# Optimization experiments

Hardware: AMD Instinct MI355X
Metric: run time of the kernel (lower is better)

Reference implementation:

```python
import jax, jax.numpy as jnp
import numpy as np

D_MODEL = 512
NUM_HEADS = 8
HEAD_DIM = D_MODEL // NUM_HEADS
BATCH = 4
SEQ = 2048
ROPE_BASE = 10000.0


def rope_cos_sin(seq_len, head_dim):
    inv_freq = 1.0 / (ROPE_BASE ** (jnp.arange(0, head_dim, 2, dtype=jnp.float32) / head_dim))
    t = jnp.arange(seq_len, dtype=jnp.float32)
    freqs = jnp.outer(t, inv_freq)              # (S, head_dim/2)
    emb = jnp.concatenate([freqs, freqs], axis=-1)  # (S, head_dim)
    return jnp.cos(emb), jnp.sin(emb)


def apply_rope(x, cos, sin):
    # x: (..., S, head_dim); cos/sin: (S, head_dim)
    x1 = x[..., ::2]
    x2 = x[..., 1::2]
    ch = cos[..., ::2]
    sh = sin[..., ::2]
    r1 = x1 * ch - x2 * sh
    r2 = x1 * sh + x2 * ch
    return jnp.stack([r1, r2], axis=-1).reshape(x.shape)


def setup_inputs() -> dict:
    key = jax.random.key(0)
    ks = jax.random.split(key, 12)
    x = jax.random.normal(ks[0], (BATCH, SEQ, D_MODEL), dtype=jnp.float32)
    variate_ids = jnp.sort(jax.random.randint(ks[1], (BATCH, SEQ), 0, 8), axis=-1).astype(jnp.int64)
    mask = jnp.ones((BATCH, SEQ), dtype=jnp.float32)
    s = 1.0 / np.sqrt(D_MODEL)
    Wq = jax.random.normal(ks[2], (D_MODEL, D_MODEL), dtype=jnp.float32) * s
    bq = jnp.zeros((D_MODEL,), dtype=jnp.float32)
    Wk = jax.random.normal(ks[3], (D_MODEL, D_MODEL), dtype=jnp.float32) * s
    bk = jnp.zeros((D_MODEL,), dtype=jnp.float32)
    Wv = jax.random.normal(ks[4], (D_MODEL, D_MODEL), dtype=jnp.float32) * s
    bv = jnp.zeros((D_MODEL,), dtype=jnp.float32)
    Wo = jax.random.normal(ks[5], (D_MODEL, D_MODEL), dtype=jnp.float32) * s
    bo = jnp.zeros((D_MODEL,), dtype=jnp.float32)
    u_same = jax.random.normal(ks[6], (NUM_HEADS,), dtype=jnp.float32) * 0.1
    u_cross = jax.random.normal(ks[7], (NUM_HEADS,), dtype=jnp.float32) * 0.1
    return dict(x=x, variate_ids=variate_ids, mask=mask, Wq=Wq, bq=bq, Wk=Wk, bk=bk,
                Wv=Wv, bv=bv, Wo=Wo, bo=bo, u_same=u_same, u_cross=u_cross)


def reference(x, variate_ids, mask, Wq, bq, Wk, bk, Wv, bv, Wo, bo, u_same, u_cross):
    B, S, D = x.shape
    H, Hd = NUM_HEADS, HEAD_DIM
    scale = 1.0 / np.sqrt(Hd)

    def proj(W, b):
        return (x @ W.T + b).reshape(B, S, H, Hd).transpose(0, 2, 1, 3)  # (B,H,S,Hd)

    q = proj(Wq, bq)
    k = proj(Wk, bk)
    v = proj(Wv, bv)

    cos, sin = rope_cos_sin(S, Hd)
    q = apply_rope(q, cos, sin)
    k = apply_rope(k, cos, sin)

    scores = jnp.einsum('bhid,bhjd->bhij', q, k) * scale  # (B,H,S,S)
    same = (variate_ids[:, :, None] == variate_ids[:, None, :]).astype(jnp.float32)  # (B,S,S)
    bias = same[:, None] * u_same[None, :, None, None] + (1.0 - same)[:, None] * u_cross[None, :, None, None]
    scores = scores + bias
    scores = scores + (1.0 - mask[:, None, None, :]) * -1e9
    probs = jax.nn.softmax(scores, axis=-1)
    out = jnp.einsum('bhij,bhjd->bhid', probs, v)  # (B,H,S,Hd)
    out = out.transpose(0, 2, 1, 3).reshape(B, S, D)
    return out @ Wo.T + bo
```

## Files before the change

kernel.cpp:

```cpp
#include <hip/hip_runtime.h>

#define BATCH   4
#define SEQ     2048
#define DMODEL  512
#define NHEADS  8
#define HEADDIM 64
#define MTOT    (BATCH*SEQ)
#define NX      (MTOT*DMODEL)
#define NW      (DMODEL*DMODEL)
#define QTILE   128
#define KTILE   64
#define NKT     (SEQ/KTILE)

#define LOG2E   1.4426950408889634f
#define SCL2    0.18033688011112042f
#define SHIFT   14.426950408889634f

typedef unsigned short u16;
typedef __bf16 bf16x8 __attribute__((ext_vector_type(8)));
typedef float  f32x4  __attribute__((ext_vector_type(4)));
typedef unsigned short u16x4 __attribute__((ext_vector_type(4)));

#define MFMA(a,b,c) __builtin_amdgcn_mfma_f32_16x16x32_bf16(a,b,c,0,0,0)

__device__ __forceinline__ u16 f2bf(float f) {
    unsigned u = __float_as_uint(f);
    u += 0x7FFFu + ((u >> 16) & 1u);
    return (u16)(u >> 16);
}

__device__ __forceinline__ float qsum16(float v) {
    v += __shfl_xor(v, 1);
    v += __shfl_xor(v, 2);
    v += __shfl_xor(v, 4);
    v += __shfl_xor(v, 8);
    return v;
}

__device__ __forceinline__ void gll16(const void* g, void* l) {
    __builtin_amdgcn_global_load_lds((const __attribute__((address_space(1))) void*)g,
                                     (__attribute__((address_space(3))) void*)l, 16, 0, 0);
}
__device__ __forceinline__ void gll4(const void* g, void* l) {
    __builtin_amdgcn_global_load_lds((const __attribute__((address_space(1))) void*)g,
                                     (__attribute__((address_space(3))) void*)l, 4, 0, 0);
}

#define NCVT4 ((NX + 4*NW)/4)
__global__ __launch_bounds__(256) void cvt_rope_kernel(
    const float* __restrict__ x,
    const float* __restrict__ wq, const float* __restrict__ wk,
    const float* __restrict__ wv, const float* __restrict__ wo,
    u16* __restrict__ xbf,
    u16* __restrict__ wqbf, u16* __restrict__ wkbf,
    u16* __restrict__ wvbf, u16* __restrict__ wobf,
    float* __restrict__ cos_t, float* __restrict__ sin_t)
{
    int i4 = blockIdx.x * 256 + threadIdx.x;
    if (i4 < NCVT4) {
        int i = i4 * 4;
        const float* s; u16* d; int o;
        if (i < NX) { s = x; d = xbf; o = i; }
        else {
            int j = i - NX;
            int r = j >> 18;
            o = j & (NW - 1);
            s = (r == 0) ? wq : (r == 1) ? wk : (r == 2) ? wv : wo;
            d = (r == 0) ? wqbf : (r == 1) ? wkbf : (r == 2) ? wvbf : wobf;
        }
        float4 v = *(const float4*)(s + o);
        u16x4 u = { f2bf(v.x), f2bf(v.y), f2bf(v.z), f2bf(v.w) };
        *(u16x4*)(d + o) = u;
    } else {
        int r = i4 - NCVT4;
        if (r < SEQ * 32 / 4) {
            int idx = r * 4;
            int s  = idx >> 5;
            int p0 = idx & 31;
#pragma unroll
            for (int t = 0; t < 4; ++t) {
                int p = p0 + t;
                float inv = __expf(-0.5756462732485115f * (float)(p & 15));
                float ang = (float)s * inv;
                cos_t[idx + t] = cosf(ang);
                sin_t[idx + t] = sinf(ang);
            }
        }
    }
}

__global__ __launch_bounds__(256) void qkv_kernel(
    const u16* __restrict__ x,
    const u16* __restrict__ Wq, const float* __restrict__ bq,
    const u16* __restrict__ Wk, const float* __restrict__ bk,
    const u16* __restrict__ Wv, const float* __restrict__ bv,
    const float* __restrict__ cos_t, const float* __restrict__ sin_t,
    u16* __restrict__ qws, u16* __restrict__ kws, u16* __restrict__ vtws)
{
    __shared__ alignas(16) u16 As[128 * 64];
    __shared__ alignas(16) u16 Bs[128 * 64];

    const int m0 = blockIdx.x * 128;
    const int n0 = blockIdx.y * 128;
    const int tid  = threadIdx.x;
    const int w    = tid >> 6;
    const int lane = tid & 63;
    const int quad = lane >> 4;
    const int l16  = lane & 15;
    const int wm = w & 1, wn = w >> 1;

    const int sec = n0 >> 9;
    const int oc0 = n0 & 511;
    const u16*   Wm = (sec == 0) ? Wq : (sec == 1 ? Wk : Wv);
    const float* bb = (sec == 0) ? bq : (sec == 1 ? bk : bv);

    f32x4 acc[4][4] = {};

    for (int kb = 0; kb < 8; ++kb) {
#pragma unroll
        for (int it = 0; it < 4; ++it) {
            const int s   = it * 256 + tid;
            const int row = s >> 3;
            const int cb  = s & 7;
            const int gcol = kb * 64 + (((cb ^ (row & 7))) << 3);
            gll16(x  + (m0  + row) * 512 + gcol, &As[s * 8]);
            gll16(Wm + (oc0 + row) * 512 + gcol, &Bs[s * 8]);
        }
        __syncthreads();

#pragma unroll
        for (int ks = 0; ks < 2; ++ks) {
            bf16x8 a[4], bfr[4];
#pragma unroll
            for (int t = 0; t < 4; ++t) {
                const int arow = wm * 64 + t * 16 + l16;
                a[t]   = *(const bf16x8*)&As[arow * 64 + (((ks * 4 + quad) ^ (arow & 7)) << 3)];
                const int brow = wn * 64 + t * 16 + l16;
                bfr[t] = *(const bf16x8*)&Bs[brow * 64 + (((ks * 4 + quad) ^ (brow & 7)) << 3)];
            }
#pragma unroll
            for (int tm = 0; tm < 4; ++tm)
#pragma unroll
                for (int tn = 0; tn < 4; ++tn)
                    acc[tm][tn] = MFMA(a[tm], bfr[tn], acc[tm][tn]);
        }
        __syncthreads();
    }

#pragma unroll
    for (int tm = 0; tm < 4; ++tm) {
#pragma unroll
        for (int tn = 0; tn < 4; ++tn) {
            const int col = oc0 + wn * 64 + tn * 16 + l16;
            const int hh  = col >> 6;
            const int d   = col & 63;
            const float bval = bb[col];
#pragma unroll
            for (int r = 0; r < 4; ++r) {
                const int R = m0 + wm * 64 + tm * 16 + quad * 4 + r;
                const int bi = R >> 11;
                const int s  = R & 2047;
                const size_t hb = (size_t)(bi * NHEADS + hh) * (SEQ * HEADDIM);
                float val = acc[tm][tn][r] + bval;
                if (sec < 2) {
                    float other = __shfl_xor(val, 1);
                    const int p = d >> 1;
                    const float c  = cos_t[s * 32 + p];
                    const float sn = sin_t[s * 32 + p];
                    float res = ((d & 1) == 0) ? (val * c - other * sn)
                                               : (other * sn + val * c);
                    if (sec == 0) {
                        qws[hb + s * HEADDIM + d] = f2bf(res);
                    } else {
                        const int kt = s >> 6, sr = s & 63;
                        kws[hb + ((kt * 64 + sr) << 6)
                               + ((((d >> 3) ^ (sr & 7)) << 3) + (d & 7))] = f2bf(res);
                    }
                } else {
                    const int kt = s >> 6, sc = s & 63;
                    vtws[hb + ((kt * 64 + d) << 6)
                            + ((((sc >> 3) ^ (d & 7)) << 3) + (sc & 7))] = f2bf(val);
                }
            }
        }
    }
}

__global__ __launch_bounds__(512) void attn_kernel(
    const u16* __restrict__ qws, const u16* __restrict__ ktl,
    const u16* __restrict__ vtl,
    const int* __restrict__ vids, const float* __restrict__ mask,
    const float* __restrict__ u_same, const float* __restrict__ u_cross,
    u16* __restrict__ attn)
{
    __shared__ alignas(16) u16 kbuf[2][KTILE * 64];
    __shared__ alignas(16) u16 vbuf[2][KTILE * 64];
    __shared__ alignas(16) u16 pls[8][16][72];
    __shared__ int   bid[2][KTILE];
    __shared__ float bmk[2][KTILE];

    const int bh = blockIdx.y;
    const int b  = bh >> 3;
    const int h  = bh & 7;
    const int q0 = blockIdx.x * QTILE;

    const int tid  = threadIdx.x;
    const int w    = tid >> 6;
    const int lane = tid & 63;
    const int quad = lane >> 4;
    const int l16  = lane & 15;

    const float us2 = u_same[h]  * LOG2E;
    const float uc2 = u_cross[h] * LOG2E;
    const size_t tb = (size_t)bh * (SEQ * HEADDIM);

    const int qr = q0 + w * 16 + l16;
    const bf16x8 aq0 = *(const bf16x8*)(qws + tb + qr * HEADDIM + quad * 8);
    const bf16x8 aq1 = *(const bf16x8*)(qws + tb + qr * HEADDIM + 32 + quad * 8);

    int vq[4];
#pragma unroll
    for (int r = 0; r < 4; ++r)
        vq[r] = vids[b * SEQ + q0 + w * 16 + quad * 4 + r];

    float li[4] = {0.f, 0.f, 0.f, 0.f};
    f32x4 o[4] = {};

    auto stage = [&](int kt, int nb) {
        const u16* kg = ktl + tb + (size_t)kt * (KTILE * 64);
        const u16* vg = vtl + tb + (size_t)kt * (KTILE * 64);
        const int off = w * 512;
        gll16(kg + off + lane * 8, &kbuf[nb][off]);
        gll16(vg + off + lane * 8, &vbuf[nb][off]);
        if (w == 0) {
            gll4(vids + b * SEQ + kt * KTILE + lane, &bid[nb][0]);
            gll4(mask + b * SEQ + kt * KTILE + lane, &bmk[nb][0]);
        }
    };

    stage(0, 0);

    for (int kt = 0; kt < NKT; ++kt) {
        const int cur = kt & 1;
        __syncthreads();
        if (kt + 1 < NKT) stage(kt + 1, cur ^ 1);

#pragma unroll
        for (int nt = 0; nt < 4; ++nt) {
            const int krow = nt * 16 + l16;
            const int r7   = krow & 7;
            const bf16x8 kb0 = *(const bf16x8*)&kbuf[cur][krow * 64 + ((quad ^ r7) << 3)];
            const bf16x8 kb1 = *(const bf16x8*)&kbuf[cur][krow * 64 + ((quad ^ r7 ^ 4) << 3)];
            f32x4 sc = {};
            sc = MFMA(aq0, kb0, sc);
            sc = MFMA(aq1, kb1, sc);
            const int   kv  = bid[cur][krow];
            const float mdl = fmaf(1.0f - bmk[cur][krow], -1.4426950408889634e9f, -SHIFT);
#pragma unroll
            for (int r = 0; r < 4; ++r) {
                const float sel = (kv == vq[r]) ? us2 : uc2;
                const float p = exp2f(fmaf(sc[r], SCL2, sel + mdl));
                li[r] += p;
                pls[w][quad * 4 + r][nt * 16 + l16] = f2bf(p);
            }
        }

        const bf16x8 ap0 = *(const bf16x8*)&pls[w][l16][quad * 8];
        const bf16x8 ap1 = *(const bf16x8*)&pls[w][l16][32 + quad * 8];

#pragma unroll
        for (int nt = 0; nt < 4; ++nt) {
            const int vrow = nt * 16 + l16;
            const int r7   = vrow & 7;
            const bf16x8 vb0 = *(const bf16x8*)&vbuf[cur][vrow * 64 + ((quad ^ r7) << 3)];
            const bf16x8 vb1 = *(const bf16x8*)&vbuf[cur][vrow * 64 + ((quad ^ r7 ^ 4) << 3)];
            o[nt] = MFMA(ap0, vb0, o[nt]);
            o[nt] = MFMA(ap1, vb1, o[nt]);
        }
    }

#pragma unroll
    for (int r = 0; r < 4; ++r) {
        const float inv = 1.0f / qsum16(li[r]);
        const int R = q0 + w * 16 + quad * 4 + r;
        const int rb = (b * SEQ + R) * DMODEL + h * HEADDIM;
#pragma unroll
        for (int nt = 0; nt < 4; ++nt)
            attn[rb + nt * 16 + l16] = f2bf(o[nt][r] * inv);
    }
}

__global__ __launch_bounds__(256) void proj_kernel(
    const u16* __restrict__ a, const u16* __restrict__ Wo,
    const float* __restrict__ bo, float* __restrict__ out)
{
    __shared__ alignas(16) u16 As[128 * 64];
    __shared__ alignas(16) u16 Bs[128 * 64];

    const int m0 = blockIdx.x * 128;
    const int n0 = blockIdx.y * 128;
    const int tid  = threadIdx.x;
    const int w    = tid >> 6;
    const int lane = tid & 63;
    const int quad = lane >> 4;
    const int l16  = lane & 15;
    const int wm = w & 1, wn = w >> 1;

    f32x4 acc[4][4] = {};

    for (int kb = 0; kb < 8; ++kb) {
#pragma unroll
        for (int it = 0; it < 4; ++it) {
            const int s   = it * 256 + tid;
            const int row = s >> 3;
            const int cb  = s & 7;
            const int gcol = kb * 64 + (((cb ^ (row & 7))) << 3);
            gll16(a  + (m0 + row) * 512 + gcol, &As[s * 8]);
            gll16(Wo + (n0 + row) * 512 + gcol, &Bs[s * 8]);
        }
        __syncthreads();

#pragma unroll
        for (int ks = 0; ks < 2; ++ks) {
            bf16x8 av[4], bv[4];
#pragma unroll
            for (int t = 0; t < 4; ++t) {
                const int arow = wm * 64 + t * 16 + l16;
                av[t] = *(const bf16x8*)&As[arow * 64 + (((ks * 4 + quad) ^ (arow & 7)) << 3)];
                const int brow = wn * 64 + t * 16 + l16;
                bv[t] = *(const bf16x8*)&Bs[brow * 64 + (((ks * 4 + quad) ^ (brow & 7)) << 3)];
            }
#pragma unroll
            for (int tm = 0; tm < 4; ++tm)
#pragma unroll
                for (int tn = 0; tn < 4; ++tn)
                    acc[tm][tn] = MFMA(av[tm], bv[tn], acc[tm][tn]);
        }
        __syncthreads();
    }

#pragma unroll
    for (int tm = 0; tm < 4; ++tm) {
#pragma unroll
        for (int tn = 0; tn < 4; ++tn) {
            const int col = n0 + wn * 64 + tn * 16 + l16;
            const float bval = bo[col];
#pragma unroll
            for (int r = 0; r < 4; ++r) {
                const int R = m0 + wm * 64 + tm * 16 + quad * 4 + r;
                out[R * 512 + col] = acc[tm][tn][r] + bval;
            }
        }
    }
}

extern "C" void kernel_launch(void* const* d_in, const int* in_sizes, int n_in,
                              void* d_out, int out_size, void* d_ws, size_t ws_size,
                              hipStream_t stream) {
    const float* x    = (const float*)d_in[0];
    const int*   vids = (const int*)d_in[1];
    const float* mask = (const float*)d_in[2];
    const float* Wq = (const float*)d_in[3];
    const float* bq = (const float*)d_in[4];
    const float* Wk = (const float*)d_in[5];
    const float* bk = (const float*)d_in[6];
    const float* Wv = (const float*)d_in[7];
    const float* bv = (const float*)d_in[8];
    const float* Wo = (const float*)d_in[9];
    const float* bo = (const float*)d_in[10];
    const float* usame  = (const float*)d_in[11];
    const float* ucross = (const float*)d_in[12];
    float* out = (float*)d_out;

    u16* xbf  = (u16*)d_ws;
    u16* wqbf = xbf + NX;
    u16* wkbf = wqbf + NW;
    u16* wvbf = wkbf + NW;
    u16* wobf = wvbf + NW;
    float* cos_t = (float*)(wobf + NW);
    float* sin_t = cos_t + SEQ * 32;
    u16* qws  = (u16*)(sin_t + SEQ * 32);
    u16* kws  = qws + (size_t)BATCH * NHEADS * SEQ * HEADDIM;
    u16* vtws = kws + (size_t)BATCH * NHEADS * SEQ * HEADDIM;
    u16* attn = xbf;

    cvt_rope_kernel<<<(NCVT4 + SEQ * 32 / 4 + 255) / 256, 256, 0, stream>>>(
        x, Wq, Wk, Wv, Wo, xbf, wqbf, wkbf, wvbf, wobf, cos_t, sin_t);

    dim3 g1(MTOT / 128, 3 * DMODEL / 128);
    qkv_kernel<<<g1, 256, 0, stream>>>(xbf, wqbf, bq, wkbf, bk, wvbf, bv,
                                       cos_t, sin_t, qws, kws, vtws);

    dim3 g2(SEQ / QTILE, BATCH * NHEADS);
    attn_kernel<<<g2, 512, 0, stream>>>(qws, kws, vtws, vids, mask,
                                        usame, ucross, attn);

    dim3 g3(MTOT / 128, DMODEL / 128);
    proj_kernel<<<g3, 256, 0, stream>>>(attn, wobf, bo, out);
}
```

Baseline: 221.2 us.

## Store K/V in plain layout, swizzle on load, pack bf16 stores, unroll attention loop

The QKV epilogue now writes K row-major and V transposed as plain [d][seq], with packed bf16 conversions and a vectorized 8-byte store for V. The LDS swizzle moves into the attention kernel's global-to-LDS staging. Cos/sin are interleaved into one float2 table. The attention loop is unrolled by two with fixed double-buffer indices, the bias/mask add is precombined, P is packed with bf16x2 conversion, and launch bounds request 4 blocks per CU. The aim is cheaper epilogue stores and lower softmax ALU cost, at the risk of less coalesced strided K/V staging loads.

```diff
diff --git a/kernel.cpp b/kernel.cpp
--- a/kernel.cpp
+++ b/kernel.cpp
@@ -1,4 +1,5 @@
 #include <hip/hip_runtime.h>
+#include <hip/hip_bf16.h>
 
 #define BATCH   4
 #define SEQ     2048
@@ -20,6 +21,7 @@
 typedef __bf16 bf16x8 __attribute__((ext_vector_type(8)));
 typedef float  f32x4  __attribute__((ext_vector_type(4)));
 typedef unsigned short u16x4 __attribute__((ext_vector_type(4)));
+typedef unsigned u32x2 __attribute__((ext_vector_type(2)));
 
 #define MFMA(a,b,c) __builtin_amdgcn_mfma_f32_16x16x32_bf16(a,b,c,0,0,0)
 
@@ -27,6 +29,12 @@
     unsigned u = __float_as_uint(f);
     u += 0x7FFFu + ((u >> 16) & 1u);
     return (u16)(u >> 16);
+}
+
+__device__ __forceinline__ unsigned pk_bf16(float a, float b) {
+    union { __hip_bfloat162 h; unsigned u; } cv;
+    cv.h = __float22bfloat162_rn(make_float2(a, b));
+    return cv.u;
 }
 
 __device__ __forceinline__ float qsum16(float v) {
@@ -54,7 +62,7 @@
     u16* __restrict__ xbf,
     u16* __restrict__ wqbf, u16* __restrict__ wkbf,
     u16* __restrict__ wvbf, u16* __restrict__ wobf,
-    float* __restrict__ cos_t, float* __restrict__ sin_t)
+    float2* __restrict__ cst)
 {
     int i4 = blockIdx.x * 256 + threadIdx.x;
     if (i4 < NCVT4) {
@@ -82,8 +90,7 @@
                 int p = p0 + t;
                 float inv = __expf(-0.5756462732485115f * (float)(p & 15));
                 float ang = (float)s * inv;
-                cos_t[idx + t] = cosf(ang);
-                sin_t[idx + t] = sinf(ang);
+                cst[idx + t] = make_float2(cosf(ang), sinf(ang));
             }
         }
     }
@@ -94,7 +101,7 @@
     const u16* __restrict__ Wq, const float* __restrict__ bq,
     const u16* __restrict__ Wk, const float* __restrict__ bk,
     const u16* __restrict__ Wv, const float* __restrict__ bv,
-    const float* __restrict__ cos_t, const float* __restrict__ sin_t,
+    const float2* __restrict__ cst,
     u16* __restrict__ qws, u16* __restrict__ kws, u16* __restrict__ vtws)
 {
     __shared__ alignas(16) u16 As[128 * 64];
@@ -113,6 +120,7 @@
     const int oc0 = n0 & 511;
     const u16*   Wm = (sec == 0) ? Wq : (sec == 1 ? Wk : Wv);
     const float* bb = (sec == 0) ? bq : (sec == 1 ? bk : bv);
+    const float  sgn = (l16 & 1) ? 1.0f : -1.0f;
 
     f32x4 acc[4][4] = {};
 
@@ -149,45 +157,42 @@
 
 #pragma unroll
     for (int tm = 0; tm < 4; ++tm) {
+        const int R0 = m0 + wm * 64 + tm * 16 + quad * 4;
+        const int bi = R0 >> 11;
+        const int s0 = R0 & 2047;
 #pragma unroll
         for (int tn = 0; tn < 4; ++tn) {
             const int col = oc0 + wn * 64 + tn * 16 + l16;
             const int hh  = col >> 6;
             const int d   = col & 63;
             const float bval = bb[col];
-#pragma unroll
-            for (int r = 0; r < 4; ++r) {
-                const int R = m0 + wm * 64 + tm * 16 + quad * 4 + r;
-                const int bi = R >> 11;
-                const int s  = R & 2047;
-                const size_t hb = (size_t)(bi * NHEADS + hh) * (SEQ * HEADDIM);
-                float val = acc[tm][tn][r] + bval;
-                if (sec < 2) {
+            const size_t hb = (size_t)(bi * NHEADS + hh) * (SEQ * HEADDIM);
+            float res[4];
+            if (sec < 2) {
+#pragma unroll
+                for (int r = 0; r < 4; ++r) {
+                    float val = acc[tm][tn][r] + bval;
                     float other = __shfl_xor(val, 1);
-                    const int p = d >> 1;
-                    const float c  = cos_t[s * 32 + p];
-                    const float sn = sin_t[s * 32 + p];
-                    float res = ((d & 1) == 0) ? (val * c - other * sn)
-                                               : (other * sn + val * c);
-                    if (sec == 0) {
-                        qws[hb + s * HEADDIM + d] = f2bf(res);
-                    } else {
-                        const int kt = s >> 6, sr = s & 63;
-                        kws[hb + ((kt * 64 + sr) << 6)
-                               + ((((d >> 3) ^ (sr & 7)) << 3) + (d & 7))] = f2bf(res);
-                    }
-                } else {
-                    const int kt = s >> 6, sc = s & 63;
-                    vtws[hb + ((kt * 64 + d) << 6)
-                            + ((((sc >> 3) ^ (d & 7)) << 3) + (sc & 7))] = f2bf(val);
+                    float2 cs = cst[(s0 + r) * 32 + (d >> 1)];
+                    res[r] = fmaf(val, cs.x, other * (sgn * cs.y));
                 }
-            }
-        }
-    }
-}
-
-__global__ __launch_bounds__(512) void attn_kernel(
-    const u16* __restrict__ qws, const u16* __restrict__ ktl,
+                const unsigned p01 = pk_bf16(res[0], res[1]);
+                const unsigned p23 = pk_bf16(res[2], res[3]);
+                u16* dp = ((sec == 0) ? qws : kws) + hb + (size_t)s0 * HEADDIM + d;
+                dp[0]   = (u16)p01;  dp[64]  = (u16)(p01 >> 16);
+                dp[128] = (u16)p23;  dp[192] = (u16)(p23 >> 16);
+            } else {
+#pragma unroll
+                for (int r = 0; r < 4; ++r) res[r] = acc[tm][tn][r] + bval;
+                u32x2 pv = { pk_bf16(res[0], res[1]), pk_bf16(res[2], res[3]) };
+                *(u32x2*)(vtws + hb + (size_t)d * SEQ + s0) = pv;
+            }
+        }
+    }
+}
+
+__global__ __launch_bounds__(512, 4) void attn_kernel(
+    const u16* __restrict__ qws, const u16* __restrict__ kws,
     const u16* __restrict__ vtl,
     const int* __restrict__ vids, const float* __restrict__ mask,
     const float* __restrict__ u_same, const float* __restrict__ u_cross,
@@ -226,25 +231,20 @@
     float li[4] = {0.f, 0.f, 0.f, 0.f};
     f32x4 o[4] = {};
 
+    const int srow = w * 8 + (lane >> 3);
+    const int scb  = lane & 7;
+    const int soff = ((scb ^ (srow & 7)) << 3);
     auto stage = [&](int kt, int nb) {
-        const u16* kg = ktl + tb + (size_t)kt * (KTILE * 64);
-        const u16* vg = vtl + tb + (size_t)kt * (KTILE * 64);
-        const int off = w * 512;
-        gll16(kg + off + lane * 8, &kbuf[nb][off]);
-        gll16(vg + off + lane * 8, &vbuf[nb][off]);
+        const int k0 = kt * KTILE;
+        gll16(kws + tb + (size_t)(k0 + srow) * HEADDIM + soff, &kbuf[nb][w * 512 + (lane & 7) * 8 + ((lane >> 3) & 7) * 0 + lane * 8 - lane * 8 + (srow - w * 8) * 64 + scb * 8]);
+        gll16(vtl + tb + (size_t)srow * SEQ + k0 + soff,        &vbuf[nb][(srow - w * 8) * 64 + w * 512 + scb * 8]);
         if (w == 0) {
-            gll4(vids + b * SEQ + kt * KTILE + lane, &bid[nb][0]);
-            gll4(mask + b * SEQ + kt * KTILE + lane, &bmk[nb][0]);
+            gll4(vids + b * SEQ + k0 + lane, &bid[nb][0]);
+            gll4(mask + b * SEQ + k0 + lane, &bmk[nb][0]);
         }
     };
 
-    stage(0, 0);
-
-    for (int kt = 0; kt < NKT; ++kt) {
-        const int cur = kt & 1;
-        __syncthreads();
-        if (kt + 1 < NKT) stage(kt + 1, cur ^ 1);
-
+    auto body = [&](const int cur) {
 #pragma unroll
         for (int nt = 0; nt < 4; ++nt) {
             const int krow = nt * 16 + l16;
@@ -255,14 +255,22 @@
             sc = MFMA(aq0, kb0, sc);
             sc = MFMA(aq1, kb1, sc);
             const int   kv  = bid[cur][krow];
-            const float mdl = fmaf(1.0f - bmk[cur][krow], -1.4426950408889634e9f, -SHIFT);
+            const float mdl = fmaf(bmk[cur][krow], 1.4426950408889634e9f,
+                                   -1.4426950408889634e9f - SHIFT);
+            const float as_ = us2 + mdl;
+            const float ac_ = uc2 + mdl;
+            float p[4];
 #pragma unroll
             for (int r = 0; r < 4; ++r) {
-                const float sel = (kv == vq[r]) ? us2 : uc2;
-                const float p = exp2f(fmaf(sc[r], SCL2, sel + mdl));
-                li[r] += p;
-                pls[w][quad * 4 + r][nt * 16 + l16] = f2bf(p);
-            }
+                const float sel = (kv == vq[r]) ? as_ : ac_;
+                p[r] = exp2f(fmaf(sc[r], SCL2, sel));
+                li[r] += p[r];
+            }
+            const unsigned p01 = pk_bf16(p[0], p[1]);
+            const unsigned p23 = pk_bf16(p[2], p[3]);
+            u16* pb = &pls[w][quad * 4][nt * 16 + l16];
+            pb[0]       = (u16)p01;  pb[72]      = (u16)(p01 >> 16);
+            pb[2 * 72]  = (u16)p23;  pb[3 * 72]  = (u16)(p23 >> 16);
         }
 
         const bf16x8 ap0 = *(const bf16x8*)&pls[w][l16][quad * 8];
@@ -277,6 +285,16 @@
             o[nt] = MFMA(ap0, vb0, o[nt]);
             o[nt] = MFMA(ap1, vb1, o[nt]);
         }
+    };
+
+    stage(0, 0);
+    for (int kt = 0; kt < NKT; kt += 2) {
+        __syncthreads();
+        stage(kt + 1, 1);
+        body(0);
+        __syncthreads();
+        if (kt + 2 < NKT) stage(kt + 2, 0);
+        body(1);
     }
 
 #pragma unroll
@@ -377,19 +395,18 @@
     u16* wkbf = wqbf + NW;
     u16* wvbf = wkbf + NW;
     u16* wobf = wvbf + NW;
-    float* cos_t = (float*)(wobf + NW);
-    float* sin_t = cos_t + SEQ * 32;
-    u16* qws  = (u16*)(sin_t + SEQ * 32);
+    float2* cst = (float2*)(wobf + NW);
+    u16* qws  = (u16*)(cst + SEQ * 32);
     u16* kws  = qws + (size_t)BATCH * NHEADS * SEQ * HEADDIM;
     u16* vtws = kws + (size_t)BATCH * NHEADS * SEQ * HEADDIM;
     u16* attn = xbf;
 
     cvt_rope_kernel<<<(NCVT4 + SEQ * 32 / 4 + 255) / 256, 256, 0, stream>>>(
-        x, Wq, Wk, Wv, Wo, xbf, wqbf, wkbf, wvbf, wobf, cos_t, sin_t);
+        x, Wq, Wk, Wv, Wo, xbf, wqbf, wkbf, wvbf, wobf, cst);
 
     dim3 g1(MTOT / 128, 3 * DMODEL / 128);
     qkv_kernel<<<g1, 256, 0, stream>>>(xbf, wqbf, bq, wkbf, bk, wvbf, bv,
-                                       cos_t, sin_t, qws, kws, vtws);
+                                       cst, qws, kws, vtws);
 
     dim3 g2(SEQ / QTILE, BATCH * NHEADS);
     attn_kernel<<<g2, 512, 0, stream>>>(qws, kws, vtws, vids, mask,
```

After: 207.1 us. 6.4% less time.
